# Performance work log

Measured on AMD Instinct MI355X. Metric: run time of the kernel, lower is better.

The kernel has to match this reference:

```python
import jax, jax.numpy as jnp
import numpy as np

H1 = 36
H2 = 1


def _lstm(x, W_ih, W_hh, b_ih, b_hh, H):
    # x: [B, T, D]; W_ih: [4H, D]; W_hh: [4H, H]; biases: [4H]
    # PyTorch gate order: i, f, g, o
    B, T, _ = x.shape
    xg = jnp.einsum('btd,gd->btg', x, W_ih) + (b_ih + b_hh)  # [B, T, 4H]

    def step(carry, xg_t):
        h, c = carry
        g = xg_t + h @ W_hh.T  # [B, 4H]
        i, f, gc, o = jnp.split(g, 4, axis=-1)
        c = jax.nn.sigmoid(f) * c + jax.nn.sigmoid(i) * jnp.tanh(gc)
        h = jax.nn.sigmoid(o) * jnp.tanh(c)
        return (h, c), h

    h0 = jnp.zeros((B, H), x.dtype)
    (_, _), hs = jax.lax.scan(step, (h0, h0), jnp.swapaxes(xg, 0, 1))
    return jnp.swapaxes(hs, 0, 1)  # [B, T, H]


def setup_inputs() -> dict:
    key = jax.random.key(0)
    ks = jax.random.split(key, 9)
    B, T = 2048, 2048
    s1 = 1.0 / np.sqrt(H1)
    s2 = 1.0  # 1/sqrt(hidden_size=1)
    return {
        'x': jax.random.normal(ks[0], (B, T, 1), dtype=jnp.float32),
        'W_ih1': jax.random.uniform(ks[1], (4 * H1, 1), jnp.float32, -s1, s1),
        'W_hh1': jax.random.uniform(ks[2], (4 * H1, H1), jnp.float32, -s1, s1),
        'b_ih1': jax.random.uniform(ks[3], (4 * H1,), jnp.float32, -s1, s1),
        'b_hh1': jax.random.uniform(ks[4], (4 * H1,), jnp.float32, -s1, s1),
        'W_ih2': jax.random.uniform(ks[5], (4 * H2, H1), jnp.float32, -s2, s2),
        'W_hh2': jax.random.uniform(ks[6], (4 * H2, H2), jnp.float32, -s2, s2),
        'b_ih2': jax.random.uniform(ks[7], (4 * H2,), jnp.float32, -s2, s2),
        'b_hh2': jax.random.uniform(ks[8], (4 * H2,), jnp.float32, -s2, s2),
    }


def reference(x, W_ih1, W_hh1, b_ih1, b_hh1, W_ih2, W_hh2, b_ih2, b_hh2):
    h1 = _lstm(x, W_ih1, W_hh1, b_ih1, b_hh1, H1)   # [B, T, 36]
    h1 = jax.nn.relu(h1)
    out = _lstm(h1, W_ih2, W_hh2, b_ih2, b_hh2, H2)  # [B, T, 1]
    return out
```

## Files before the change

kernel.cpp:

```cpp
#include <hip/hip_runtime.h>

namespace {

constexpr int T_LEN = 2048;
constexpr int B_TOT = 2048;
constexpr int H1 = 36;
constexpr int NB = 16;
constexpr int BLOCK = 640;
constexpr int RS = 80;

typedef _Float16 f16x8 __attribute__((ext_vector_type(8)));
typedef _Float16 h16x2 __attribute__((ext_vector_type(2)));
typedef float f32x4 __attribute__((ext_vector_type(4)));

__device__ __forceinline__ float fdot2(float wb, float hb, float acc) {
#if __has_builtin(__builtin_amdgcn_fdot2)
  return __builtin_amdgcn_fdot2(__builtin_bit_cast(h16x2, wb),
                                __builtin_bit_cast(h16x2, hb), acc, false);
#else
  float d;
  asm("v_dot2_f32_f16 %0, %1, %2, %3" : "=v"(d) : "v"(wb), "v"(hb), "0"(acc));
  return d;
#endif
}
__device__ __forceinline__ float pack2h(float a, float b) {
  h16x2 t = {(_Float16)a, (_Float16)b};
  return __builtin_bit_cast(float, t);
}
template <int PAT>
__device__ __forceinline__ float swzf(float v) {
  return __builtin_bit_cast(
      float, __builtin_amdgcn_ds_swizzle(__builtin_bit_cast(int, v), PAT));
}
__device__ __forceinline__ float fexp2(float x) { return __builtin_amdgcn_exp2f(x); }
__device__ __forceinline__ float frcp(float x) { return __builtin_amdgcn_rcpf(x); }
__device__ __forceinline__ float sigm(float x) { return frcp(1.f + fexp2(x * -1.44269504f)); }
__device__ __forceinline__ float tanh_fast(float x) {
  return fmaf(2.f, frcp(1.f + fexp2(x * -2.88539008f)), -1.f);
}

__global__ __launch_bounds__(BLOCK) void lstm2_kernel(
    const float* __restrict__ x, const float* __restrict__ Wih1,
    const float* __restrict__ Whh1, const float* __restrict__ bih1,
    const float* __restrict__ bhh1, const float* __restrict__ Wih2,
    const float* __restrict__ Whh2, const float* __restrict__ bih2,
    const float* __restrict__ bhh2, float* __restrict__ out)
{
  __shared__ __align__(16) _Float16 lds[2][2][NB][RS];

  const int tid = threadIdx.x;
  const int wid = tid >> 6;
  const int lane = tid & 63;
  const int g0 = blockIdx.x * NB;
  const bool isA = wid < 9;

  for (int i = tid; i < 2 * 2 * NB * RS; i += BLOCK)
    ((_Float16*)lds)[i] = (_Float16)0.f;
  __syncthreads();

  const int m = lane & 15;
  const int q = lane >> 4;
  f16x8 A0 = {}, A1 = {};
  float wxc[4] = {0, 0, 0, 0}, bxc[4] = {0, 0, 0, 0};
  float c1 = 0.f;
  const float* xc = nullptr;
  if (isA) {
    const int u0 = wid * 4;
    const int ra = (m & 3) * H1 + (u0 + (m >> 2));
#pragma unroll
    for (int j = 0; j < 8; ++j) {
      A0[j] = (_Float16)Whh1[ra * H1 + q * 8 + j];
      const int k1 = 32 + q * 8 + j;
      A1[j] = (k1 < H1) ? (_Float16)Whh1[ra * H1 + k1] : (_Float16)0.f;
    }
#pragma unroll
    for (int r = 0; r < 4; ++r) {
      const int rc = r * H1 + (u0 + q);
      wxc[r] = Wih1[rc];
      bxc[r] = bih1[rc] + bhh1[rc];
    }
    xc = x + (size_t)(g0 + m) * T_LEN;
  }

  const int lb = lane >> 2, lg = lane & 3;
  float w2[18];
  float whg = 0.f, b2 = 0.f, c2 = 0.f, h2 = 0.f;
  float* outp = nullptr;
#pragma unroll
  for (int k = 0; k < 18; ++k) w2[k] = 0.f;
  if (!isA) {
    const float* wr = Wih2 + lg * H1;
#pragma unroll
    for (int k = 0; k < 18; ++k) w2[k] = pack2h(wr[2 * k], wr[2 * k + 1]);
    whg = Whh2[lg];
    b2 = bih2[lg] + bhh2[lg];
    outp = out + (size_t)(g0 + lb) * T_LEN;
  }

  float4 qx = make_float4(0.f, 0.f, 0.f, 0.f);
  if (isA) qx = *(const float4*)xc;
  float4 ov = make_float4(0.f, 0.f, 0.f, 0.f);

  auto step = [&](int i, float xv, int s) {
    const int ib = (s + 1) & 1;
    const int wb = s & 1;
    if (isA) {
      const f16x8 B0 = *(const f16x8*)&lds[ib][0][m][q * 8];
      const f16x8 B1 = *(const f16x8*)&lds[ib][0][m][32 + q * 8];
      f32x4 cc;
#pragma unroll
      for (int r = 0; r < 4; ++r) cc[r] = fmaf(xv, wxc[r], bxc[r]);
      cc = __builtin_amdgcn_mfma_f32_16x16x32_f16(A0, B0, cc, 0, 0, 0);
      cc = __builtin_amdgcn_mfma_f32_16x16x32_f16(A1, B1, cc, 0, 0, 0);
      const float I = sigm(cc[0]), F = sigm(cc[1]);
      const float G = tanh_fast(cc[2]), O = sigm(cc[3]);
      c1 = fmaf(F, c1, I * G);
      const float h = O * tanh_fast(c1);
      const int ku = (wid << 2) + q;
      lds[wb][0][m][ku] = (_Float16)h;
      lds[wb][1][m][ku] = (_Float16)fmaxf(h, 0.f);
    } else if (i > 0) {
      const char* rp = (const char*)&lds[ib][1][lb][0];
      const float4 r0 = *(const float4*)rp;
      const float4 r1 = *(const float4*)(rp + 16);
      const float4 r2 = *(const float4*)(rp + 32);
      const float4 r3 = *(const float4*)(rp + 48);
      const float2 r4 = *(const float2*)(rp + 64);
      const float f[18] = {r0.x, r0.y, r0.z, r0.w, r1.x, r1.y, r1.z, r1.w,
                           r2.x, r2.y, r2.z, r2.w, r3.x, r3.y, r3.z, r3.w,
                           r4.x, r4.y};
      float aE = 0.f, aO = 0.f;
#pragma unroll
      for (int k = 0; k < 18; k += 2) aE = fdot2(w2[k], f[k], aE);
#pragma unroll
      for (int k = 1; k < 18; k += 2) aO = fdot2(w2[k], f[k], aO);
      const float pre = (aE + aO) + fmaf(h2, whg, b2);
      const float pI = swzf<0x8000 | 0x00>(pre);
      const float pF = swzf<0x8000 | 0x55>(pre);
      const float pG = swzf<0x8000 | 0xAA>(pre);
      const float pO = swzf<0x8000 | 0xFF>(pre);
      c2 = fmaf(sigm(pF), c2, sigm(pI) * tanh_fast(pG));
      h2 = sigm(pO) * tanh_fast(c2);
      if (s == 1) ov.x = h2;
      else if (s == 2) ov.y = h2;
      else if (s == 3) ov.z = h2;
      else {
        ov.w = h2;
        if (lg == 0) *(float4*)(outp + (i - 4)) = ov;
      }
    }
    __syncthreads();
  };

  for (int i0 = 0; i0 < T_LEN; i0 += 4) {
    float4 qn = qx;
    if (isA) {
      const int tn = (i0 + 4 < T_LEN) ? (i0 + 4) : (T_LEN - 4);
      qn = *(const float4*)(xc + tn);
    }
    step(i0 + 0, qx.x, 0);
    step(i0 + 1, qx.y, 1);
    step(i0 + 2, qx.z, 2);
    step(i0 + 3, qx.w, 3);
    qx = qn;
  }
  step(T_LEN, qx.x, 0);
}

}

extern "C" void kernel_launch(void* const* d_in, const int* in_sizes, int n_in,
                              void* d_out, int out_size, void* d_ws, size_t ws_size,
                              hipStream_t stream) {
  const float* x    = (const float*)d_in[0];
  const float* Wih1 = (const float*)d_in[1];
  const float* Whh1 = (const float*)d_in[2];
  const float* bih1 = (const float*)d_in[3];
  const float* bhh1 = (const float*)d_in[4];
  const float* Wih2 = (const float*)d_in[5];
  const float* Whh2 = (const float*)d_in[6];
  const float* bih2 = (const float*)d_in[7];
  const float* bhh2 = (const float*)d_in[8];
  float* out = (float*)d_out;

  dim3 grid(B_TOT / NB);
  dim3 block(BLOCK);
  hipLaunchKernelGGL(lstm2_kernel, grid, block, 0, stream,
                     x, Wih1, Whh1, bih1, bhh1, Wih2, Whh2, bih2, bhh2, out);
}
```

Baseline: 912.4 us.

## Shrink blocks to four sequences with three waves covering all layer-1 units

```diff
diff --git a/kernel.cpp b/kernel.cpp
--- a/kernel.cpp
+++ b/kernel.cpp
@@ -5,9 +5,9 @@
 constexpr int T_LEN = 2048;
 constexpr int B_TOT = 2048;
 constexpr int H1 = 36;
-constexpr int NB = 16;
-constexpr int BLOCK = 640;
-constexpr int RS = 80;
+constexpr int NB = 4;
+constexpr int BLOCK = 256;
+constexpr int RS = 72;
 
 typedef _Float16 f16x8 __attribute__((ext_vector_type(8)));
 typedef _Float16 h16x2 __attribute__((ext_vector_type(2)));
@@ -26,6 +26,11 @@
 __device__ __forceinline__ float pack2h(float a, float b) {
   h16x2 t = {(_Float16)a, (_Float16)b};
   return __builtin_bit_cast(float, t);
+}
+__device__ __forceinline__ float pkmax0(float v, float z) {
+  float d;
+  asm("v_pk_max_f16 %0, %1, %2" : "=v"(d) : "v"(v), "v"(z));
+  return d;
 }
 template <int PAT>
 __device__ __forceinline__ float swzf(float v) {
@@ -46,49 +51,51 @@
     const float* __restrict__ Whh2, const float* __restrict__ bih2,
     const float* __restrict__ bhh2, float* __restrict__ out)
 {
-  __shared__ __align__(16) _Float16 lds[2][2][NB][RS];
+  __shared__ __align__(16) _Float16 lds[2][16][RS];
 
   const int tid = threadIdx.x;
   const int wid = tid >> 6;
   const int lane = tid & 63;
   const int g0 = blockIdx.x * NB;
-  const bool isA = wid < 9;
+  const bool isA = wid < 3;
 
-  for (int i = tid; i < 2 * 2 * NB * RS; i += BLOCK)
-    ((_Float16*)lds)[i] = (_Float16)0.f;
+  for (int i = tid; i < 2 * 16 * RS; i += BLOCK) ((_Float16*)lds)[i] = (_Float16)0.f;
   __syncthreads();
 
   const int m = lane & 15;
   const int q = lane >> 4;
-  f16x8 A0 = {}, A1 = {};
-  float wxc[4] = {0, 0, 0, 0}, bxc[4] = {0, 0, 0, 0};
-  float c1 = 0.f;
+  f16x8 A0[3] = {}, A1[3] = {};
+  float wxc[3][4] = {}, bxc[3][4] = {};
+  float c1[3] = {0.f, 0.f, 0.f};
   const float* xc = nullptr;
   if (isA) {
-    const int u0 = wid * 4;
-    const int ra = (m & 3) * H1 + (u0 + (m >> 2));
 #pragma unroll
-    for (int j = 0; j < 8; ++j) {
-      A0[j] = (_Float16)Whh1[ra * H1 + q * 8 + j];
-      const int k1 = 32 + q * 8 + j;
-      A1[j] = (k1 < H1) ? (_Float16)Whh1[ra * H1 + k1] : (_Float16)0.f;
+    for (int j = 0; j < 3; ++j) {
+      const int u0 = 4 * (wid * 3 + j);
+      const int ra = (m & 3) * H1 + (u0 + (m >> 2));
+#pragma unroll
+      for (int jj = 0; jj < 8; ++jj) {
+        A0[j][jj] = (_Float16)Whh1[ra * H1 + q * 8 + jj];
+        const int k1 = 32 + q * 8 + jj;
+        A1[j][jj] = (k1 < H1) ? (_Float16)Whh1[ra * H1 + k1] : (_Float16)0.f;
+      }
+#pragma unroll
+      for (int r = 0; r < 4; ++r) {
+        const int rc = r * H1 + (u0 + q);
+        wxc[j][r] = Wih1[rc];
+        bxc[j][r] = bih1[rc] + bhh1[rc];
+      }
     }
-#pragma unroll
-    for (int r = 0; r < 4; ++r) {
-      const int rc = r * H1 + (u0 + q);
-      wxc[r] = Wih1[rc];
-      bxc[r] = bih1[rc] + bhh1[rc];
-    }
-    xc = x + (size_t)(g0 + m) * T_LEN;
+    xc = x + (size_t)(g0 + (m < NB ? m : NB - 1)) * T_LEN;
   }
 
   const int lb = lane >> 2, lg = lane & 3;
   float w2[18];
-  float whg = 0.f, b2 = 0.f, c2 = 0.f, h2 = 0.f;
+  float whg = 0.f, b2 = 0.f, c2 = 0.f, h2 = 0.f, zero = 0.f;
   float* outp = nullptr;
 #pragma unroll
   for (int k = 0; k < 18; ++k) w2[k] = 0.f;
-  if (!isA) {
+  if (!isA && lane < 16) {
     const float* wr = Wih2 + lg * H1;
 #pragma unroll
     for (int k = 0; k < 18; ++k) w2[k] = pack2h(wr[2 * k], wr[2 * k + 1]);
@@ -105,35 +112,36 @@
     const int ib = (s + 1) & 1;
     const int wb = s & 1;
     if (isA) {
-      const f16x8 B0 = *(const f16x8*)&lds[ib][0][m][q * 8];
-      const f16x8 B1 = *(const f16x8*)&lds[ib][0][m][32 + q * 8];
-      f32x4 cc;
+      const f16x8 B0 = *(const f16x8*)&lds[ib][m][q * 8];
+      const f16x8 B1 = *(const f16x8*)&lds[ib][m][32 + q * 8];
 #pragma unroll
-      for (int r = 0; r < 4; ++r) cc[r] = fmaf(xv, wxc[r], bxc[r]);
-      cc = __builtin_amdgcn_mfma_f32_16x16x32_f16(A0, B0, cc, 0, 0, 0);
-      cc = __builtin_amdgcn_mfma_f32_16x16x32_f16(A1, B1, cc, 0, 0, 0);
-      const float I = sigm(cc[0]), F = sigm(cc[1]);
-      const float G = tanh_fast(cc[2]), O = sigm(cc[3]);
-      c1 = fmaf(F, c1, I * G);
-      const float h = O * tanh_fast(c1);
-      const int ku = (wid << 2) + q;
-      lds[wb][0][m][ku] = (_Float16)h;
-      lds[wb][1][m][ku] = (_Float16)fmaxf(h, 0.f);
-    } else if (i > 0) {
-      const char* rp = (const char*)&lds[ib][1][lb][0];
+      for (int j = 0; j < 3; ++j) {
+        f32x4 cc;
+#pragma unroll
+        for (int r = 0; r < 4; ++r) cc[r] = fmaf(xv, wxc[j][r], bxc[j][r]);
+        cc = __builtin_amdgcn_mfma_f32_16x16x32_f16(A0[j], B0, cc, 0, 0, 0);
+        cc = __builtin_amdgcn_mfma_f32_16x16x32_f16(A1[j], B1, cc, 0, 0, 0);
+        const float I = sigm(cc[0]), F = sigm(cc[1]);
+        const float G = tanh_fast(cc[2]), O = sigm(cc[3]);
+        c1[j] = fmaf(F, c1[j], I * G);
+        const float h = O * tanh_fast(c1[j]);
+        if (m < NB) lds[wb][m][4 * (wid * 3 + j) + q] = (_Float16)h;
+      }
+    } else if (i > 0 && lane < 16) {
+      const char* rp = (const char*)&lds[ib][lb][0];
       const float4 r0 = *(const float4*)rp;
       const float4 r1 = *(const float4*)(rp + 16);
       const float4 r2 = *(const float4*)(rp + 32);
       const float4 r3 = *(const float4*)(rp + 48);
       const float2 r4 = *(const float2*)(rp + 64);
-      const float f[18] = {r0.x, r0.y, r0.z, r0.w, r1.x, r1.y, r1.z, r1.w,
-                           r2.x, r2.y, r2.z, r2.w, r3.x, r3.y, r3.z, r3.w,
-                           r4.x, r4.y};
+      float f[18] = {r0.x, r0.y, r0.z, r0.w, r1.x, r1.y, r1.z, r1.w,
+                     r2.x, r2.y, r2.z, r2.w, r3.x, r3.y, r3.z, r3.w,
+                     r4.x, r4.y};
       float aE = 0.f, aO = 0.f;
 #pragma unroll
-      for (int k = 0; k < 18; k += 2) aE = fdot2(w2[k], f[k], aE);
+      for (int k = 0; k < 18; k += 2) aE = fdot2(w2[k], pkmax0(f[k], zero), aE);
 #pragma unroll
-      for (int k = 1; k < 18; k += 2) aO = fdot2(w2[k], f[k], aO);
+      for (int k = 1; k < 18; k += 2) aO = fdot2(w2[k], pkmax0(f[k], zero), aO);
       const float pre = (aE + aO) + fmaf(h2, whg, b2);
       const float pI = swzf<0x8000 | 0x00>(pre);
       const float pF = swzf<0x8000 | 0x55>(pre);
```

Result: slower. 1.456 ms (+59.5%).

## Halve batch rows per block and apply ReLU in the layer-2 consumer

Applied to the files above, without the earlier changes.

```diff
diff --git a/kernel.cpp b/kernel.cpp
--- a/kernel.cpp
+++ b/kernel.cpp
@@ -5,9 +5,9 @@
 constexpr int T_LEN = 2048;
 constexpr int B_TOT = 2048;
 constexpr int H1 = 36;
-constexpr int NB = 16;
+constexpr int NB = 8;
 constexpr int BLOCK = 640;
-constexpr int RS = 80;
+constexpr int RS = 72;
 
 typedef _Float16 f16x8 __attribute__((ext_vector_type(8)));
 typedef _Float16 h16x2 __attribute__((ext_vector_type(2)));
@@ -26,6 +26,11 @@
 __device__ __forceinline__ float pack2h(float a, float b) {
   h16x2 t = {(_Float16)a, (_Float16)b};
   return __builtin_bit_cast(float, t);
+}
+__device__ __forceinline__ float pkmax0(float v, float z) {
+  float d;
+  asm("v_pk_max_f16 %0, %1, %2" : "=v"(d) : "v"(v), "v"(z));
+  return d;
 }
 template <int PAT>
 __device__ __forceinline__ float swzf(float v) {
@@ -46,7 +51,7 @@
     const float* __restrict__ Whh2, const float* __restrict__ bih2,
     const float* __restrict__ bhh2, float* __restrict__ out)
 {
-  __shared__ __align__(16) _Float16 lds[2][2][NB][RS];
+  __shared__ __align__(16) _Float16 lds[2][16][RS];
 
   const int tid = threadIdx.x;
   const int wid = tid >> 6;
@@ -54,8 +59,7 @@
   const int g0 = blockIdx.x * NB;
   const bool isA = wid < 9;
 
-  for (int i = tid; i < 2 * 2 * NB * RS; i += BLOCK)
-    ((_Float16*)lds)[i] = (_Float16)0.f;
+  for (int i = tid; i < 2 * 16 * RS; i += BLOCK) ((_Float16*)lds)[i] = (_Float16)0.f;
   __syncthreads();
 
   const int m = lane & 15;
@@ -79,12 +83,12 @@
       wxc[r] = Wih1[rc];
       bxc[r] = bih1[rc] + bhh1[rc];
     }
-    xc = x + (size_t)(g0 + m) * T_LEN;
+    xc = x + (size_t)(g0 + (m < NB ? m : NB - 1)) * T_LEN;
   }
 
   const int lb = lane >> 2, lg = lane & 3;
   float w2[18];
-  float whg = 0.f, b2 = 0.f, c2 = 0.f, h2 = 0.f;
+  float whg = 0.f, b2 = 0.f, c2 = 0.f, h2 = 0.f, zero = 0.f;
   float* outp = nullptr;
 #pragma unroll
   for (int k = 0; k < 18; ++k) w2[k] = 0.f;
@@ -94,7 +98,7 @@
     for (int k = 0; k < 18; ++k) w2[k] = pack2h(wr[2 * k], wr[2 * k + 1]);
     whg = Whh2[lg];
     b2 = bih2[lg] + bhh2[lg];
-    outp = out + (size_t)(g0 + lb) * T_LEN;
+    outp = out + (size_t)(g0 + (lb < NB ? lb : NB - 1)) * T_LEN;
   }
 
   float4 qx = make_float4(0.f, 0.f, 0.f, 0.f);
@@ -105,8 +109,8 @@
     const int ib = (s + 1) & 1;
     const int wb = s & 1;
     if (isA) {
-      const f16x8 B0 = *(const f16x8*)&lds[ib][0][m][q * 8];
-      const f16x8 B1 = *(const f16x8*)&lds[ib][0][m][32 + q * 8];
+      const f16x8 B0 = *(const f16x8*)&lds[ib][m][q * 8];
+      const f16x8 B1 = *(const f16x8*)&lds[ib][m][32 + q * 8];
       f32x4 cc;
 #pragma unroll
       for (int r = 0; r < 4; ++r) cc[r] = fmaf(xv, wxc[r], bxc[r]);
@@ -116,11 +120,9 @@
       const float G = tanh_fast(cc[2]), O = sigm(cc[3]);
       c1 = fmaf(F, c1, I * G);
       const float h = O * tanh_fast(c1);
-      const int ku = (wid << 2) + q;
-      lds[wb][0][m][ku] = (_Float16)h;
-      lds[wb][1][m][ku] = (_Float16)fmaxf(h, 0.f);
+      lds[wb][m][(wid << 2) + q] = (_Float16)h;
     } else if (i > 0) {
-      const char* rp = (const char*)&lds[ib][1][lb][0];
+      const char* rp = (const char*)&lds[ib][lb][0];
       const float4 r0 = *(const float4*)rp;
       const float4 r1 = *(const float4*)(rp + 16);
       const float4 r2 = *(const float4*)(rp + 32);
@@ -131,9 +133,9 @@
                            r4.x, r4.y};
       float aE = 0.f, aO = 0.f;
 #pragma unroll
-      for (int k = 0; k < 18; k += 2) aE = fdot2(w2[k], f[k], aE);
+      for (int k = 0; k < 18; k += 2) aE = fdot2(w2[k], pkmax0(f[k], zero), aE);
 #pragma unroll
-      for (int k = 1; k < 18; k += 2) aO = fdot2(w2[k], f[k], aO);
+      for (int k = 1; k < 18; k += 2) aO = fdot2(w2[k], pkmax0(f[k], zero), aO);
       const float pre = (aE + aO) + fmaf(h2, whg, b2);
       const float pI = swzf<0x8000 | 0x00>(pre);
       const float pF = swzf<0x8000 | 0x55>(pre);
@@ -146,7 +148,7 @@
       else if (s == 3) ov.z = h2;
       else {
         ov.w = h2;
-        if (lg == 0) *(float4*)(outp + (i - 4)) = ov;
+        if (lg == 0 && lb < NB) *(float4*)(outp + (i - 4)) = ov;
       }
     }
     __syncthreads();
```

New measurement: 979.5 us. +7.4%, slower.
